# Optimization experiments

Hardware: AMD Instinct MI355X
Metric: run time of the kernel (lower is better)

Reference implementation:

```python
import jax, jax.numpy as jnp
import numpy as np

HEADS = 4
KS = 7  # neighborhood window size


def group_norm(x, g, b, eps=1e-5):
    # GroupNorm(1, C) on NCHW: normalize over (C,H,W) per sample
    mu = x.mean(axis=(1, 2, 3), keepdims=True)
    var = x.var(axis=(1, 2, 3), keepdims=True)
    xn = (x - mu) * jax.lax.rsqrt(var + eps)
    return xn * g[None, :, None, None] + b[None, :, None, None]


def layer_norm(x, g, b, eps=1e-5):
    mu = x.mean(axis=-1, keepdims=True)
    var = x.var(axis=-1, keepdims=True)
    return (x - mu) * jax.lax.rsqrt(var + eps) * g + b


def na2d(x, qkv_w, qkv_b, proj_w, proj_b, rpb):
    # Neighborhood attention 2D (NATTEN semantics: window clamped at borders)
    N, H, W, C = x.shape
    e, k = HEADS, KS
    d = C // e
    qkv = x @ qkv_w.T + qkv_b  # [N,H,W,3C]
    q, kk, v = jnp.split(qkv, 3, axis=-1)
    q = q.reshape(N, H, W, e, d) * (d ** -0.5)
    kk = kk.reshape(N, H, W, e, d)
    v = v.reshape(N, H, W, e, d)
    ni = jnp.clip(jnp.arange(H) - k // 2, 0, H - k)[:, None] + jnp.arange(k)  # [H,k]
    nj = jnp.clip(jnp.arange(W) - k // 2, 0, W - k)[:, None] + jnp.arange(k)  # [W,k]
    kg = kk[:, ni][:, :, :, nj]  # [N,H,i,W,j,e,d]
    vg = v[:, ni][:, :, :, nj]
    scores = jnp.einsum('nhwed,nhiwjed->nhweij', q, kg)  # [N,H,W,e,k,k]
    ri = ni - jnp.arange(H)[:, None] + (k - 1)  # rel pos index in [0, 2k-2]
    rj = nj - jnp.arange(W)[:, None] + (k - 1)
    bias = rpb[:, ri][:, :, :, rj]  # [e,H,i,W,j]
    scores = scores + bias.transpose(1, 3, 0, 2, 4)[None]
    attn = jax.nn.softmax(scores.reshape(N, H, W, e, k * k), axis=-1).reshape(N, H, W, e, k, k)
    out = jnp.einsum('nhweij,nhiwjed->nhwed', attn, vg).reshape(N, H, W, C)
    return out @ proj_w.T + proj_b


def na_layer(x, gn_g, gn_b, qkv_w, qkv_b, proj_w, proj_b, rpb, ln_g, ln_b, fc1_w, fc1_b, fc2_w, fc2_b):
    N, C, H, W = x.shape
    x1 = x.transpose(0, 2, 3, 1)  # n h w c (pre-norm residual)
    xg = group_norm(x, gn_g, gn_b).transpose(0, 2, 3, 1)
    a = na2d(xg, qkv_w, qkv_b, proj_w, proj_b, rpb) + x1
    t = a.reshape(N, H * W, C)
    h = jax.nn.gelu(layer_norm(t, ln_g, ln_b) @ fc1_w.T + fc1_b, approximate=False)
    t = t + (h @ fc2_w.T + fc2_b)
    return t.reshape(N, H, W, C).transpose(0, 3, 1, 2)


def conv3x3(x, w, b):
    y = jax.lax.conv_general_dilated(x, w, (1, 1), 'SAME', dimension_numbers=('NCHW', 'OIHW', 'NCHW'))
    return y + b[None, :, None, None]


def setup_inputs() -> dict:
    key = jax.random.key(0)
    ks = jax.random.split(key, 16)
    N, C, H, W = 2, 128, 64, 64
    L, e, k, hid, red = 2, HEADS, KS, 4 * 128, 18
    rn = lambda kk, shape, s=0.02: jax.random.normal(kk, shape, jnp.float32) * s
    return {
        'x': jax.random.normal(ks[0], (N, C, H, W), jnp.float32),
        'gn_g': jnp.ones((L, C), jnp.float32), 'gn_b': jnp.zeros((L, C), jnp.float32),
        'qkv_w': rn(ks[1], (L, 3 * C, C)), 'qkv_b': jnp.zeros((L, 3 * C), jnp.float32),
        'proj_w': rn(ks[2], (L, C, C)), 'proj_b': jnp.zeros((L, C), jnp.float32),
        'rpb': rn(ks[3], (L, e, 2 * k - 1, 2 * k - 1)),
        'ln_g': jnp.ones((L, C), jnp.float32), 'ln_b': jnp.zeros((L, C), jnp.float32),
        'fc1_w': rn(ks[4], (L, hid, C)), 'fc1_b': jnp.zeros((L, hid), jnp.float32),
        'fc2_w': rn(ks[5], (L, C, hid)), 'fc2_b': jnp.zeros((L, C), jnp.float32),
        'bconv_w': rn(ks[6], (C, C, 3, 3)), 'bconv_b': jnp.zeros((C,), jnp.float32),
        'c1_w': rn(ks[7], (C // 4, C)), 'c1_b': jnp.zeros((C // 4,), jnp.float32),
        'c2_w': rn(ks[8], (C, C // 4)), 'c2_b': jnp.zeros((C,), jnp.float32),
        'ca1_w': rn(ks[9], (C // red, C)), 'ca1_b': jnp.zeros((C // red,), jnp.float32),
        'ca2_w': rn(ks[10], (C, C // red)), 'ca2_b': jnp.zeros((C,), jnp.float32),
    }


def reference(x, gn_g, gn_b, qkv_w, qkv_b, proj_w, proj_b, rpb, ln_g, ln_b, fc1_w, fc1_b, fc2_w, fc2_b, bconv_w, bconv_b, c1_w, c1_b, c2_w, c2_b, ca1_w, ca1_b, ca2_w, ca2_b):
    res = x
    for l in range(gn_g.shape[0]):  # n_resblocks (structurally fixed, small)
        res = na_layer(res, gn_g[l], gn_b[l], qkv_w[l], qkv_b[l], proj_w[l], proj_b[l], rpb[l],
                       ln_g[l], ln_b[l], fc1_w[l], fc1_b[l], fc2_w[l], fc2_b[l])
    res = conv3x3(res, bconv_w, bconv_b)
    # tail: 1x1 conv -> ReLU -> 1x1 conv -> CALayer
    y = jax.nn.relu(jnp.einsum('rc,nchw->nrhw', c1_w, res) + c1_b[None, :, None, None])
    y = jnp.einsum('cr,nrhw->nchw', c2_w, y) + c2_b[None, :, None, None]
    p = y.mean(axis=(2, 3))  # global avg pool -> [N,C]
    s = jax.nn.sigmoid(jax.nn.relu(p @ ca1_w.T + ca1_b) @ ca2_w.T + ca2_b)
    y = y * s[:, :, None, None]
    return y + x
```

## Files before the change

### kernel.cpp

```cpp
#include <hip/hip_runtime.h>
#include <math.h>

typedef unsigned short u16;

#define NN 2
#define CC 128
#define HH 64
#define WW 64
#define NHD 4
#define DH 32
#define KSZ 7
#define PIX (NN*HH*WW)
#define HID 512
#define C4 32
#define CRED 7
#define RW 22
#define RNB 160
#define NBV 154

typedef float f32x4 __attribute__((ext_vector_type(4)));
typedef short bf16x8 __attribute__((ext_vector_type(8)));

static __device__ __forceinline__ float u2f(u16 u){ return __uint_as_float(((unsigned)u) << 16); }
static __device__ __forceinline__ u16 f2u(float f){
    unsigned b = __float_as_uint(f);
    return (u16)((b + 0x7FFFu + ((b >> 16) & 1u)) >> 16);
}

__global__ void detect_k(const u16* __restrict__ x, int* __restrict__ flag,
                         float* __restrict__ poolacc){
    __shared__ float red[256];
    int t = threadIdx.x;
    float mx = 0.f;
    for(int i = t; i < 4096; i += 256){
        float v = fabsf(u2f(x[i]));
        if(v < 1e30f) mx = fmaxf(mx, v);
    }
    red[t] = mx; __syncthreads();
    for(int s = 128; s > 0; s >>= 1){
        if(t < s) red[t] = fmaxf(red[t], red[t+s]);
        __syncthreads();
    }
    if(t == 0) *flag = (red[0] > 1e6f) ? 1 : 0;
    if(t < NN*CC) poolacc[t] = 0.f;
}

struct PtrTab { const void* p[23]; int off[24]; };
#define NCVT 2172
#define NRPK 576
#define NNCH 512

__global__ __launch_bounds__(256) void setup_k(
    PtrTab tab, u16* __restrict__ Wb, u16* __restrict__ Wt,
    const void* __restrict__ convw, const void* __restrict__ x,
    float* __restrict__ cur, float* __restrict__ part,
    const int* __restrict__ flag, int total)
{
    int blk = blockIdx.x;
    int t = threadIdx.x;
    int fl = *flag;
    if(blk < NCVT){
        int i = blk*256 + t;
        if(i < total){
            int a = 0;
            while(i >= tab.off[a+1]) a++;
            int loc = i - tab.off[a];
            Wb[i] = fl ? f2u(((const float*)tab.p[a])[loc]) : ((const u16*)tab.p[a])[loc];
        }
        return;
    }
    if(blk < NCVT + NRPK){
        int i = (blk - NCVT)*256 + t;
        if(i < CC*CC*9){
            int o = i/(9*CC); int rem = i%(9*CC); int tap = rem/CC; int c = rem%CC;
            size_t s = (size_t)(o*CC + c)*9 + tap;
            Wt[i] = fl ? f2u(((const float*)convw)[s]) : ((const u16*)convw)[s];
        }
        return;
    }
    __shared__ float tile[32][65];
    __shared__ float wred[4][2];
    int u = blk - NCVT - NRPK;
    int bx = u & 3, by = u >> 2;
    int n = by >> 6, i = by & 63;
    for(int idx = t; idx < 32*64; idx += 256){
        int cl = idx >> 6, j = idx & 63;
        size_t src = ((size_t)(n*CC + bx*32 + cl)*HH + i)*WW + j;
        tile[cl][j] = fl ? ((const float*)x)[src] : u2f(((const u16*)x)[src]);
    }
    __syncthreads();
    float s = 0.f, q = 0.f;
    for(int idx = t; idx < 64*32; idx += 256){
        int j = idx >> 5, cl = idx & 31;
        float v = tile[cl][j];
        cur[((size_t)((n*HH + i)*WW) + j)*CC + bx*32 + cl] = v;
        s += v; q += v*v;
    }
    #pragma unroll
    for(int off = 32; off > 0; off >>= 1){ s += __shfl_xor(s, off, 64); q += __shfl_xor(q, off, 64); }
    int wave = t >> 6;
    if((t & 63) == 0){ wred[wave][0] = s; wred[wave][1] = q; }
    __syncthreads();
    if(t == 0){
        float ss = wred[0][0]+wred[1][0]+wred[2][0]+wred[3][0];
        float qq = wred[0][1]+wred[1][1]+wred[2][1]+wred[3][1];
        int pidx = n*256 + i*4 + bx;
        part[pidx*2] = ss; part[pidx*2+1] = qq;
    }
}

enum { EPI_NONE = 0, EPI_RES = 1, EPI_GELU = 2 };
enum { OUT_F32 = 0, OUT_BF16 = 1, OUT_BOTH = 2 };
enum { EX_NONE = 0, EX_STATS = 1 };
#define LDP 136

template<int EPI, int OUTM, int AGN, int EXTRA>
__global__ __launch_bounds__(256) void g64_k(
    const void* __restrict__ Av, const u16* __restrict__ W, const u16* __restrict__ bias,
    const float* __restrict__ R, float* __restrict__ Cf, u16* __restrict__ Cb,
    const u16* __restrict__ gnw, const u16* __restrict__ gnb,
    float* __restrict__ gnpart, int gncount,
    int M, int N, int K)
{
    __shared__ __align__(16) u16 As[64*LDP];
    __shared__ __align__(16) u16 Bs[64*LDP];
    __shared__ float wred[4][2];
    const int bm = blockIdx.y*64, bn = blockIdx.x*64;
    const int t = threadIdx.x;
    const int wave = t >> 6, lane = t & 63;
    const int wm = (wave >> 1)*32, wn = (wave & 1)*32;
    const int lg = lane >> 4, lr = lane & 15;
    const int nsm = bm >> 12;
    f32x4 acc[2][2];
    #pragma unroll
    for(int i = 0; i < 2; i++)
        #pragma unroll
        for(int j = 0; j < 2; j++) acc[i][j] = (f32x4){0.f,0.f,0.f,0.f};

    float gmu = 0.f, grs = 0.f;
    if(AGN){
        float a = 0.f, q = 0.f;
        for(int idx = lane; idx < gncount; idx += 64){
            a += gnpart[(nsm*gncount + idx)*2];
            q += gnpart[(nsm*gncount + idx)*2 + 1];
        }
        #pragma unroll
        for(int off = 32; off > 0; off >>= 1){
            a += __shfl_xor(a, off, 64); q += __shfl_xor(q, off, 64);
        }
        const float inv = 1.f/(float)(HH*WW*CC);
        gmu = a*inv;
        grs = rsqrtf(fmaxf(q*inv - gmu*gmu, 0.f) + 1e-5f);
    }

    for(int k0 = 0; k0 < K; k0 += 128){
        uint4 ra[4], rb[4];
        float4 fa[4][2];
        #pragma unroll
        for(int r = 0; r < 4; r++){
            int e = r*256 + t;
            int row = e >> 4, ch = e & 15;
            if(AGN){
                const float* ap = (const float*)Av + (size_t)(bm+row)*K + k0 + ch*8;
                fa[r][0] = *(const float4*)ap;
                fa[r][1] = *(const float4*)(ap + 4);
            } else {
                ra[r] = *(const uint4*)((const u16*)Av + (size_t)(bm+row)*K + k0 + ch*8);
            }
            rb[r] = (bn+row < N) ? *(const uint4*)(W + (size_t)(bn+row)*K + k0 + ch*8)
                                 : (uint4){0,0,0,0};
        }
        #pragma unroll
        for(int r = 0; r < 4; r++){
            int e = r*256 + t;
            int row = e >> 4, ch = e & 15;
            if(AGN){
                union { uint4 u; u16 h[8]; } g8, b8, o8;
                g8.u = *(const uint4*)(gnw + k0 + ch*8);
                b8.u = *(const uint4*)(gnb + k0 + ch*8);
                const float* fv = (const float*)&fa[r][0];
                #pragma unroll
                for(int z = 0; z < 8; z++)
                    o8.h[z] = f2u((fv[z]-gmu)*grs*u2f(g8.h[z]) + u2f(b8.h[z]));
                *(uint4*)&As[row*LDP + ch*8] = o8.u;
            } else {
                *(uint4*)&As[row*LDP + ch*8] = ra[r];
            }
            *(uint4*)&Bs[row*LDP + ch*8] = rb[r];
        }
        __syncthreads();
        #pragma unroll
        for(int kc = 0; kc < 4; kc++){
            bf16x8 af0 = *(const bf16x8*)&As[(wm + lr)*LDP      + kc*32 + lg*8];
            bf16x8 af1 = *(const bf16x8*)&As[(wm + 16 + lr)*LDP + kc*32 + lg*8];
            bf16x8 bf0 = *(const bf16x8*)&Bs[(wn + lr)*LDP      + kc*32 + lg*8];
            bf16x8 bf1 = *(const bf16x8*)&Bs[(wn + 16 + lr)*LDP + kc*32 + lg*8];
            acc[0][0] = __builtin_amdgcn_mfma_f32_16x16x32_bf16(af0, bf0, acc[0][0], 0, 0, 0);
            acc[0][1] = __builtin_amdgcn_mfma_f32_16x16x32_bf16(af0, bf1, acc[0][1], 0, 0, 0);
            acc[1][0] = __builtin_amdgcn_mfma_f32_16x16x32_bf16(af1, bf0, acc[1][0], 0, 0, 0);
            acc[1][1] = __builtin_amdgcn_mfma_f32_16x16x32_bf16(af1, bf1, acc[1][1], 0, 0, 0);
        }
        if(k0 + 128 < K) __syncthreads();
    }

    float ssum = 0.f, sq = 0.f;
    #pragma unroll
    for(int i = 0; i < 2; i++){
        #pragma unroll
        for(int j = 0; j < 2; j++){
            int col = bn + wn + j*16 + lr;
            if(col >= N) continue;
            #pragma unroll
            for(int reg = 0; reg < 4; reg++){
                int row = bm + wm + i*16 + lg*4 + reg;
                float v = acc[i][j][reg] + u2f(bias[col]);
                if(EPI == EPI_RES)  v += R[(size_t)row*N + col];
                if(EPI == EPI_GELU) v = 0.5f*v*(1.f + erff(v*0.70710678118f));
                if(OUTM == OUT_F32 || OUTM == OUT_BOTH) Cf[(size_t)row*N + col] = v;
                if(OUTM == OUT_BF16 || OUTM == OUT_BOTH) Cb[(size_t)row*N + col] = f2u(v);
                if(EXTRA == EX_STATS){ ssum += v; sq += v*v; }
            }
        }
    }
    if(EXTRA == EX_STATS){
        #pragma unroll
        for(int off = 32; off > 0; off >>= 1){
            ssum += __shfl_xor(ssum, off, 64); sq += __shfl_xor(sq, off, 64);
        }
        if(lane == 0){ wred[wave][0] = ssum; wred[wave][1] = sq; }
        __syncthreads();
        if(t == 0){
            int bidx = blockIdx.y*gridDim.x + blockIdx.x;
            gnpart[bidx*2]   = wred[0][0]+wred[1][0]+wred[2][0]+wred[3][0];
            gnpart[bidx*2+1] = wred[0][1]+wred[1][1]+wred[2][1]+wred[3][1];
        }
    }
}

__global__ __launch_bounds__(256) void proj_ln_k(
    const u16* __restrict__ A, const u16* __restrict__ W, const u16* __restrict__ bias,
    const float* __restrict__ R, const u16* __restrict__ lng, const u16* __restrict__ lnb,
    float* __restrict__ abuf, u16* __restrict__ lnout)
{
    __shared__ __align__(16) u16 As[32*LDP];
    __shared__ __align__(16) u16 Bs[128*LDP];
    __shared__ float redS[32][2], redQ[32][2], muS[32], rsS[32];
    const int bm = blockIdx.x*32;
    const int t = threadIdx.x;
    const int wave = t >> 6, lane = t & 63;
    const int wm = (wave >> 1)*16, wn = (wave & 1)*64;
    const int lg = lane >> 4, lr = lane & 15;

    {
        uint4 ra[2], rb[8];
        #pragma unroll
        for(int r = 0; r < 2; r++){
            int e = r*256 + t; int row = e >> 4, ch = e & 15;
            ra[r] = *(const uint4*)(A + (size_t)(bm+row)*CC + ch*8);
        }
        #pragma unroll
        for(int r = 0; r < 8; r++){
            int e = r*256 + t; int row = e >> 4, ch = e & 15;
            rb[r] = *(const uint4*)(W + (size_t)row*CC + ch*8);
        }
        #pragma unroll
        for(int r = 0; r < 2; r++){
            int e = r*256 + t; int row = e >> 4, ch = e & 15;
            *(uint4*)&As[row*LDP + ch*8] = ra[r];
        }
        #pragma unroll
        for(int r = 0; r < 8; r++){
            int e = r*256 + t; int row = e >> 4, ch = e & 15;
            *(uint4*)&Bs[row*LDP + ch*8] = rb[r];
        }
    }
    __syncthreads();

    f32x4 acc[4];
    #pragma unroll
    for(int j = 0; j < 4; j++) acc[j] = (f32x4){0.f,0.f,0.f,0.f};
    #pragma unroll
    for(int kc = 0; kc < 4; kc++){
        bf16x8 af = *(const bf16x8*)&As[(wm + lr)*LDP + kc*32 + lg*8];
        #pragma unroll
        for(int j = 0; j < 4; j++){
            bf16x8 bf = *(const bf16x8*)&Bs[(wn + j*16 + lr)*LDP + kc*32 + lg*8];
            acc[j] = __builtin_amdgcn_mfma_f32_16x16x32_bf16(af, bf, acc[j], 0, 0, 0);
        }
    }
    #pragma unroll
    for(int reg = 0; reg < 4; reg++){
        int rl = wm + lg*4 + reg;
        float rs_ = 0.f, rq_ = 0.f;
        #pragma unroll
        for(int j = 0; j < 4; j++){
            int col = wn + j*16 + lr;
            float v = acc[j][reg] + u2f(bias[col]) + R[(size_t)(bm+rl)*CC + col];
            acc[j][reg] = v;
            abuf[(size_t)(bm+rl)*CC + col] = v;
            rs_ += v; rq_ += v*v;
        }
        rs_ += __shfl_xor(rs_, 1, 64); rq_ += __shfl_xor(rq_, 1, 64);
        rs_ += __shfl_xor(rs_, 2, 64); rq_ += __shfl_xor(rq_, 2, 64);
        rs_ += __shfl_xor(rs_, 4, 64); rq_ += __shfl_xor(rq_, 4, 64);
        rs_ += __shfl_xor(rs_, 8, 64); rq_ += __shfl_xor(rq_, 8, 64);
        if(lr == 0){ redS[rl][wn>>6] = rs_; redQ[rl][wn>>6] = rq_; }
    }
    __syncthreads();
    if(t < 32){
        float mu = (redS[t][0] + redS[t][1])*(1.f/CC);
        float var = fmaxf((redQ[t][0] + redQ[t][1])*(1.f/CC) - mu*mu, 0.f);
        muS[t] = mu; rsS[t] = rsqrtf(var + 1e-5f);
    }
    __syncthreads();
    #pragma unroll
    for(int reg = 0; reg < 4; reg++){
        int rl = wm + lg*4 + reg;
        float mu = muS[rl], rstd = rsS[rl];
        #pragma unroll
        for(int j = 0; j < 4; j++){
            int col = wn + j*16 + lr;
            float v = (acc[j][reg] - mu)*rstd*u2f(lng[col]) + u2f(lnb[col]);
            lnout[(size_t)(bm+rl)*CC + col] = f2u(v);
        }
    }
}

__global__ __launch_bounds__(256) void mct_k(
    const u16* __restrict__ in, const u16* __restrict__ Wt, const u16* __restrict__ bias,
    const u16* __restrict__ c1w, const u16* __restrict__ c1b,
    const u16* __restrict__ c2w, const u16* __restrict__ c2b,
    float* __restrict__ ybuf, float* __restrict__ poolacc)
{
    __shared__ __align__(16) u16 As[16*LDP];
    __shared__ __align__(16) u16 Bs[128*LDP];
    u16* Bs1 = Bs;
    u16* Bs2 = Bs + 32*LDP;
    u16* Hs  = Bs + 32*LDP + 128*40;
    const int bm = blockIdx.x*16;
    const int t = threadIdx.x;
    const int wave = t >> 6, lane = t & 63;
    const int wn = wave*32;
    const int lg = lane >> 4, lr = lane & 15;
    const int nsm = bm >> 12;

    uint4 rb1[2], rb2[2];
    #pragma unroll
    for(int r = 0; r < 2; r++){
        int e = r*256 + t; int row = e >> 4, ch = e & 15;
        rb1[r] = *(const uint4*)(c1w + (size_t)row*CC + ch*8);
    }
    #pragma unroll
    for(int r = 0; r < 2; r++){
        int e = r*256 + t; int row = e >> 2, ch = e & 3;
        rb2[r] = *(const uint4*)(c2w + (size_t)row*C4 + ch*8);
    }

    f32x4 acc[2];
    acc[0] = (f32x4){0.f,0.f,0.f,0.f}; acc[1] = (f32x4){0.f,0.f,0.f,0.f};

    for(int tap = 0; tap < 9; tap++){
        int dy = tap/3 - 1, dx = tap%3 - 1;
        uint4 ra, rb[8];
        {
            int row = t >> 4, ch = t & 15;
            int p = bm + row;
            int n = p >> 12, ii = (p & 4095) >> 6, jj = p & 63;
            int y = ii + dy, x = jj + dx;
            ra = (uint4){0,0,0,0};
            if(y >= 0 && y < HH && x >= 0 && x < WW)
                ra = *(const uint4*)(in + (size_t)(((n*HH + y)*WW + x))*CC + ch*8);
        }
        #pragma unroll
        for(int r = 0; r < 8; r++){
            int e = r*256 + t; int row = e >> 4, ch = e & 15;
            rb[r] = *(const uint4*)(Wt + (size_t)row*(9*CC) + tap*128 + ch*8);
        }
        {
            int row = t >> 4, ch = t & 15;
            *(uint4*)&As[row*LDP + ch*8] = ra;
        }
        #pragma unroll
        for(int r = 0; r < 8; r++){
            int e = r*256 + t; int row = e >> 4, ch = e & 15;
            *(uint4*)&Bs[row*LDP + ch*8] = rb[r];
        }
        __syncthreads();
        #pragma unroll
        for(int kc = 0; kc < 4; kc++){
            bf16x8 af = *(const bf16x8*)&As[lr*LDP + kc*32 + lg*8];
            #pragma unroll
            for(int j = 0; j < 2; j++){
                bf16x8 bf = *(const bf16x8*)&Bs[(wn + j*16 + lr)*LDP + kc*32 + lg*8];
                acc[j] = __builtin_amdgcn_mfma_f32_16x16x32_bf16(af, bf, acc[j], 0, 0, 0);
            }
        }
        __syncthreads();
    }

    #pragma unroll
    for(int j = 0; j < 2; j++){
        int col = wn + j*16 + lr;
        #pragma unroll
        for(int reg = 0; reg < 4; reg++){
            int rl = lg*4 + reg;
            As[rl*LDP + col] = f2u(acc[j][reg] + u2f(bias[col]));
        }
    }
    #pragma unroll
    for(int r = 0; r < 2; r++){
        int e = r*256 + t; int row = e >> 4, ch = e & 15;
        *(uint4*)&Bs1[row*LDP + ch*8] = rb1[r];
    }
    #pragma unroll
    for(int r = 0; r < 2; r++){
        int e = r*256 + t; int row = e >> 2, ch = e & 3;
        *(uint4*)&Bs2[row*40 + ch*8] = rb2[r];
    }
    __syncthreads();

    {
        const int wn1 = (wave & 1)*16;
        f32x4 a1 = (f32x4){0.f,0.f,0.f,0.f};
        #pragma unroll
        for(int kc = 0; kc < 4; kc++){
            bf16x8 af = *(const bf16x8*)&As[lr*LDP + kc*32 + lg*8];
            bf16x8 bf = *(const bf16x8*)&Bs1[(wn1 + lr)*LDP + kc*32 + lg*8];
            a1 = __builtin_amdgcn_mfma_f32_16x16x32_bf16(af, bf, a1, 0, 0, 0);
        }
        #pragma unroll
        for(int reg = 0; reg < 4; reg++){
            int rl = lg*4 + reg;
            int col = wn1 + lr;
            Hs[rl*40 + col] = f2u(fmaxf(a1[reg] + u2f(c1b[col]), 0.f));
        }
    }
    __syncthreads();

    {
        f32x4 a2[2];
        a2[0] = (f32x4){0.f,0.f,0.f,0.f}; a2[1] = (f32x4){0.f,0.f,0.f,0.f};
        bf16x8 af = *(const bf16x8*)&Hs[lr*40 + lg*8];
        #pragma unroll
        for(int j = 0; j < 2; j++){
            bf16x8 bf = *(const bf16x8*)&Bs2[(wn + j*16 + lr)*40 + lg*8];
            a2[j] = __builtin_amdgcn_mfma_f32_16x16x32_bf16(af, bf, a2[j], 0, 0, 0);
        }
        float cs[2] = {0.f, 0.f};
        #pragma unroll
        for(int j = 0; j < 2; j++){
            int col = wn + j*16 + lr;
            #pragma unroll
            for(int reg = 0; reg < 4; reg++){
                int row = bm + lg*4 + reg;
                float v = a2[j][reg] + u2f(c2b[col]);
                ybuf[(size_t)row*CC + col] = v;
                cs[j] += v;
            }
        }
        #pragma unroll
        for(int j = 0; j < 2; j++){
            cs[j] += __shfl_xor(cs[j], 16, 64);
            cs[j] += __shfl_xor(cs[j], 32, 64);
        }
        if(lg == 0){
            #pragma unroll
            for(int j = 0; j < 2; j++)
                atomicAdd(&poolacc[nsm*CC + wn + j*16 + lr], cs[j]);
        }
    }
}

#define KVP 72
#define PSP 168

__global__ __launch_bounds__(128) void att_tile_k(
    const u16* __restrict__ qkv, const u16* __restrict__ rpb, u16* __restrict__ out)
{
    __shared__ __align__(16) u16 KV[2][RNB][KVP];
    __shared__ __align__(16) u16 Qs[16][64];
    __shared__ float rpbs[2][169];
    u16* PsB = &KV[0][0][0];
    const int blk = blockIdx.x;
    const int rb = blk >> 1, eg = blk & 1;
    const int p0 = rb*16;
    const int jb = p0 & 63, i = (p0 >> 6) & 63, n = p0 >> 12;
    const int i0 = min(max(i-3, 0), HH-KSZ);
    const int rc0 = min(max(jb-3, 0), WW-KSZ);
    const int t = threadIdx.x;

    for(int idx = t; idx < 2*169; idx += 128)
        rpbs[idx/169][idx%169] = u2f(rpb[(eg*2 + idx/169)*169 + idx%169]);
    {
        int pix = t >> 3, ch = t & 7;
        *(uint4*)&Qs[pix][ch*8] = *(const uint4*)(qkv + (size_t)(p0+pix)*(3*CC) + eg*64 + ch*8);
    }
    for(int idx = t; idx < RNB*16; idx += 128){
        int nb = idx >> 4, part = idx & 15;
        int kv = part >> 3, ch = part & 7;
        uint4 v = (uint4){0,0,0,0};
        if(nb < NBV){
            int ky = nb/RW, kcol = nb - ky*RW;
            int sy = i0 + ky, sx = min(rc0 + kcol, WW-1);
            v = *(const uint4*)(qkv + (size_t)((n*HH + sy)*WW + sx)*(3*CC) + CC + kv*CC + eg*64 + ch*8);
        }
        *(uint4*)&KV[kv][nb][ch*8] = v;
    }
    __syncthreads();

    const int el = t >> 6;
    const int lane = t & 63, lg = lane >> 4, lr = lane & 15;

    bf16x8 aq = *(const bf16x8*)&Qs[lr][el*32 + lg*8];
    f32x4 sc[10];
    #pragma unroll
    for(int c = 0; c < 10; c++){
        bf16x8 bk = *(const bf16x8*)&KV[0][c*16+lr][el*32 + lg*8];
        sc[c] = __builtin_amdgcn_mfma_f32_16x16x32_bf16(aq, bk, (f32x4){0.f,0.f,0.f,0.f}, 0, 0, 0);
    }
    __syncthreads();
    #pragma unroll
    for(int reg = 0; reg < 4; reg++){
        int pix = lg*4 + reg;
        int j = jb + pix;
        int base = min(max(j-3, 0), WW-KSZ) - rc0;
        float mx = -1e30f;
        #pragma unroll
        for(int c = 0; c < 10; c++){
            int nb = c*16 + lr;
            int ky = nb/RW, kcol = nb - ky*RW;
            float v = -1e30f;
            if(nb < NBV && kcol >= base && kcol <= base+6){
                int ri = i0 + ky - i + (KSZ-1);
                int rj = rc0 + kcol - j + (KSZ-1);
                v = sc[c][reg]*0.17677669529663689f + rpbs[el][ri*13 + rj];
            }
            sc[c][reg] = v;
            mx = fmaxf(mx, v);
        }
        mx = fmaxf(mx, __shfl_xor(mx, 1, 64));
        mx = fmaxf(mx, __shfl_xor(mx, 2, 64));
        mx = fmaxf(mx, __shfl_xor(mx, 4, 64));
        mx = fmaxf(mx, __shfl_xor(mx, 8, 64));
        float sum = 0.f;
        #pragma unroll
        for(int c = 0; c < 10; c++){
            float p = __expf(sc[c][reg] - mx);
            sc[c][reg] = p; sum += p;
        }
        sum += __shfl_xor(sum, 1, 64);
        sum += __shfl_xor(sum, 2, 64);
        sum += __shfl_xor(sum, 4, 64);
        sum += __shfl_xor(sum, 8, 64);
        float rs = 1.f/sum;
        #pragma unroll
        for(int c = 0; c < 10; c++)
            PsB[(el*16 + pix)*PSP + c*16 + lr] = f2u(sc[c][reg]*rs);
    }
    __syncthreads();
    f32x4 o0 = (f32x4){0.f,0.f,0.f,0.f}, o1 = (f32x4){0.f,0.f,0.f,0.f};
    #pragma unroll
    for(int ks = 0; ks < 5; ks++){
        bf16x8 ap = *(const bf16x8*)&PsB[(el*16 + lr)*PSP + ks*32 + lg*8];
        bf16x8 b0, b1;
        #pragma unroll
        for(int jj = 0; jj < 8; jj++){
            int nb = ks*32 + lg*8 + jj;
            b0[jj] = (short)KV[1][nb][el*32 + lr];
            b1[jj] = (short)KV[1][nb][el*32 + 16 + lr];
        }
        o0 = __builtin_amdgcn_mfma_f32_16x16x32_bf16(ap, b0, o0, 0, 0, 0);
        o1 = __builtin_amdgcn_mfma_f32_16x16x32_bf16(ap, b1, o1, 0, 0, 0);
    }
    int e = eg*2 + el;
    #pragma unroll
    for(int reg = 0; reg < 4; reg++){
        int pix = lg*4 + reg;
        out[(size_t)(p0+pix)*CC + e*32 + lr]      = f2u(o0[reg]);
        out[(size_t)(p0+pix)*CC + e*32 + 16 + lr] = f2u(o1[reg]);
    }
}

__global__ __launch_bounds__(256) void final_ca_k(
    const float* __restrict__ y, const float* __restrict__ poolacc,
    const u16* __restrict__ w1, const u16* __restrict__ b1,
    const u16* __restrict__ w2, const u16* __restrict__ b2,
    const void* __restrict__ xraw, void* __restrict__ outv,
    const int* __restrict__ flag)
{
    __shared__ float t1s[CRED];
    __shared__ float sres;
    int id0 = blockIdx.x*256;
    int c = (id0 >> 12) & (CC-1);
    int n = id0 >> 19;
    int t = threadIdx.x;
    if(t < CRED){
        float a = u2f(b1[t]);
        const float pscale = 1.f/(float)(HH*WW);
        for(int cc = 0; cc < CC; cc++)
            a += poolacc[n*CC + cc]*pscale*u2f(w1[t*CC + cc]);
        t1s[t] = fmaxf(a, 0.f);
    }
    __syncthreads();
    if(t == 0){
        float a = u2f(b2[c]);
        #pragma unroll
        for(int r = 0; r < CRED; r++) a += t1s[r]*u2f(w2[c*CRED + r]);
        sres = 1.f/(1.f + __expf(-a));
    }
    __syncthreads();
    float s = sres;
    int id = id0 + t;
    int j = id & 63; int i = (id >> 6) & 63;
    float xr = (*flag) ? ((const float*)xraw)[id] : u2f(((const u16*)xraw)[id]);
    float v = y[(size_t)((n*HH + i)*WW + j)*CC + c]*s + xr;
    if(*flag) ((float*)outv)[id] = v;
    else      ((u16*)outv)[id] = f2u(v);
}

extern "C" void kernel_launch(void* const* d_in, const int* in_sizes, int n_in,
                              void* d_out, int out_size, void* d_ws, size_t ws_size,
                              hipStream_t stream){
    float* wsf    = (float*)d_ws;
    int*   flagp  = (int*)d_ws;
    float* gnpart = wsf + 8;
    float* poolacc= wsf + 1040;

    u16* Wb = (u16*)(wsf + 2048);
    static const int wsizes[23] = {256,256,98304,768,32768,256,1352,256,256,131072,1024,
                                   131072,256,147456,128,4096,32,4096,128,896,7,896,128};
    int woff[24]; woff[0] = 0;
    for(int i = 0; i < 23; i++) woff[i+1] = woff[i] + wsizes[i];
    const int WTOT = woff[23];
    u16* Wt = Wb + 555760;

    float* AB    = wsf + 360448;
    float* cur   = AB;
    u16*  cur16  = (u16*)(AB + 1048576);
    u16*  xg16   = (u16*)(AB + 1572864);
    u16*  qkv16  = (u16*)(AB + 2097152);
    float* abuf  = AB + 2097152;
    u16*  hbuf16 = (u16*)(AB + 3670016);
    float* ybuf  = AB + 3670016;

    detect_k<<<1, 256, 0, stream>>>((const u16*)d_in[0], flagp, poolacc);

    PtrTab tab;
    for(int i = 0; i < 23; i++){ tab.p[i] = d_in[i+1]; tab.off[i] = woff[i]; }
    tab.off[23] = woff[23];
    setup_k<<<NCVT + NRPK + NNCH, 256, 0, stream>>>(
        tab, Wb, Wt, d_in[14], d_in[0], cur, gnpart, flagp, WTOT);

    const u16 *gng = Wb+woff[0], *gnb = Wb+woff[1], *qkvw = Wb+woff[2], *qkvb = Wb+woff[3],
              *projw = Wb+woff[4], *projb = Wb+woff[5], *rpbw = Wb+woff[6], *lng = Wb+woff[7],
              *lnb = Wb+woff[8], *f1w = Wb+woff[9], *f1b = Wb+woff[10], *f2w = Wb+woff[11],
              *f2b = Wb+woff[12], *bcb = Wb+woff[14], *c1w = Wb+woff[15],
              *c1b = Wb+woff[16], *c2w = Wb+woff[17], *c2b = Wb+woff[18], *ca1w = Wb+woff[19],
              *ca1b = Wb+woff[20], *ca2w = Wb+woff[21], *ca2b = Wb+woff[22];

    for(int l = 0; l < 2; l++){
        int gncount = (l == 0) ? 256 : 128;

        g64_k<EPI_NONE,OUT_BF16,1,EX_NONE><<<dim3(6, PIX/64), 256, 0, stream>>>(
            cur, qkvw + (size_t)l*3*CC*CC, qkvb + l*3*CC, nullptr, nullptr, qkv16,
            gng + l*CC, gnb + l*CC, gnpart, gncount, PIX, 3*CC, CC);

        att_tile_k<<<PIX/16*2, 128, 0, stream>>>(qkv16, rpbw + l*NHD*169, xg16);

        proj_ln_k<<<PIX/32, 256, 0, stream>>>(
            xg16, projw + (size_t)l*CC*CC, projb + l*CC, cur, lng + l*CC, lnb + l*CC,
            abuf, xg16);

        g64_k<EPI_GELU,OUT_BF16,0,EX_NONE><<<dim3(8, PIX/64), 256, 0, stream>>>(
            xg16, f1w + (size_t)l*HID*CC, f1b + l*HID, nullptr, nullptr, hbuf16,
            nullptr, nullptr, nullptr, 0, PIX, HID, CC);

        g64_k<EPI_RES,OUT_BOTH,0,EX_STATS><<<dim3(2, PIX/64), 256, 0, stream>>>(
            hbuf16, f2w + (size_t)l*CC*HID, f2b + l*CC, abuf, cur, cur16,
            nullptr, nullptr, gnpart, 0, PIX, CC, HID);
    }

    mct_k<<<PIX/16, 256, 0, stream>>>(cur16, Wt, bcb, c1w, c1b, c2w, c2b, ybuf, poolacc);

    final_ca_k<<<(NN*CC*HH*WW)/256, 256, 0, stream>>>(
        ybuf, poolacc, ca1w, ca1b, ca2w, ca2b, d_in[0], d_out, flagp);
}
```

Baseline: 263.6 us.

## Fold input-format detection into setup kernel and add smaller-tile fc2 GEMM kernel

Removes the separate single-block detect kernel by having every setup block recompute the bf16/f32 flag from the first 256 input elements with a wave reduction. Block 0 writes the flag and zeroes the pool accumulator. The fc2 GEMM moves to a dedicated kernel with 32x64 tiles, which doubles the grid to raise occupancy for the K=512 reduction. That kernel fuses the residual add, the dual f32/bf16 outputs and the GroupNorm partial statistics, so the per-layer GN count is now always 256. The risks are a redundant per-block reduction in setup, a flag that now depends on only 256 samples instead of 4096, and a smaller tile that reuses less data from LDS.

After: 268.4 us. No clear change (+1.8%).

```diff
diff --git a/kernel.cpp b/kernel.cpp
--- a/kernel.cpp
+++ b/kernel.cpp
@@ -27,24 +27,6 @@
     return (u16)((b + 0x7FFFu + ((b >> 16) & 1u)) >> 16);
 }
 
-__global__ void detect_k(const u16* __restrict__ x, int* __restrict__ flag,
-                         float* __restrict__ poolacc){
-    __shared__ float red[256];
-    int t = threadIdx.x;
-    float mx = 0.f;
-    for(int i = t; i < 4096; i += 256){
-        float v = fabsf(u2f(x[i]));
-        if(v < 1e30f) mx = fmaxf(mx, v);
-    }
-    red[t] = mx; __syncthreads();
-    for(int s = 128; s > 0; s >>= 1){
-        if(t < s) red[t] = fmaxf(red[t], red[t+s]);
-        __syncthreads();
-    }
-    if(t == 0) *flag = (red[0] > 1e6f) ? 1 : 0;
-    if(t < NN*CC) poolacc[t] = 0.f;
-}
-
 struct PtrTab { const void* p[23]; int off[24]; };
 #define NCVT 2172
 #define NRPK 576
@@ -54,11 +36,25 @@
     PtrTab tab, u16* __restrict__ Wb, u16* __restrict__ Wt,
     const void* __restrict__ convw, const void* __restrict__ x,
     float* __restrict__ cur, float* __restrict__ part,
-    const int* __restrict__ flag, int total)
+    int* __restrict__ flagp, float* __restrict__ poolacc, int total)
 {
-    int blk = blockIdx.x;
-    int t = threadIdx.x;
-    int fl = *flag;
+    __shared__ float red4[4];
+    const int blk = blockIdx.x, t = threadIdx.x;
+
+    {
+        float v = fabsf(u2f(((const u16*)x)[t]));
+        float mx = (v < 1e30f) ? v : 0.f;
+        #pragma unroll
+        for(int off = 32; off > 0; off >>= 1) mx = fmaxf(mx, __shfl_xor(mx, off, 64));
+        if((t & 63) == 0) red4[t >> 6] = mx;
+    }
+    __syncthreads();
+    const int fl = (fmaxf(fmaxf(red4[0], red4[1]), fmaxf(red4[2], red4[3])) > 1e6f) ? 1 : 0;
+    if(blk == 0){
+        if(t == 0) *flagp = fl;
+        if(t < NN*CC) poolacc[t] = 0.f;
+    }
+
     if(blk < NCVT){
         int i = blk*256 + t;
         if(i < total){
@@ -203,7 +199,6 @@
         if(k0 + 128 < K) __syncthreads();
     }
 
-    float ssum = 0.f, sq = 0.f;
     #pragma unroll
     for(int i = 0; i < 2; i++){
         #pragma unroll
@@ -218,22 +213,87 @@
                 if(EPI == EPI_GELU) v = 0.5f*v*(1.f + erff(v*0.70710678118f));
                 if(OUTM == OUT_F32 || OUTM == OUT_BOTH) Cf[(size_t)row*N + col] = v;
                 if(OUTM == OUT_BF16 || OUTM == OUT_BOTH) Cb[(size_t)row*N + col] = f2u(v);
-                if(EXTRA == EX_STATS){ ssum += v; sq += v*v; }
             }
         }
     }
-    if(EXTRA == EX_STATS){
-        #pragma unroll
-        for(int off = 32; off > 0; off >>= 1){
-            ssum += __shfl_xor(ssum, off, 64); sq += __shfl_xor(sq, off, 64);
-        }
-        if(lane == 0){ wred[wave][0] = ssum; wred[wave][1] = sq; }
+    (void)wred;
+}
+
+__global__ __launch_bounds__(256) void fc2_k(
+    const u16* __restrict__ A, const u16* __restrict__ W, const u16* __restrict__ bias,
+    const float* __restrict__ R, float* __restrict__ Cf, u16* __restrict__ Cb,
+    float* __restrict__ gnpart)
+{
+    __shared__ __align__(16) u16 As[32*LDP];
+    __shared__ __align__(16) u16 Bs[64*LDP];
+    __shared__ float wred[4][2];
+    const int bm = blockIdx.y*32, bn = blockIdx.x*64;
+    const int t = threadIdx.x;
+    const int wave = t >> 6, lane = t & 63;
+    const int wm = (wave >> 1)*16, wn = (wave & 1)*32;
+    const int lg = lane >> 4, lr = lane & 15;
+    const int nsm = bm >> 12;
+    f32x4 acc[2];
+    acc[0] = (f32x4){0.f,0.f,0.f,0.f}; acc[1] = (f32x4){0.f,0.f,0.f,0.f};
+
+    for(int k0 = 0; k0 < HID; k0 += 128){
+        uint4 ra[2], rb[4];
+        #pragma unroll
+        for(int r = 0; r < 2; r++){
+            int e = r*256 + t; int row = e >> 4, ch = e & 15;
+            ra[r] = *(const uint4*)(A + (size_t)(bm+row)*HID + k0 + ch*8);
+        }
+        #pragma unroll
+        for(int r = 0; r < 4; r++){
+            int e = r*256 + t; int row = e >> 4, ch = e & 15;
+            rb[r] = *(const uint4*)(W + (size_t)(bn+row)*HID + k0 + ch*8);
+        }
+        #pragma unroll
+        for(int r = 0; r < 2; r++){
+            int e = r*256 + t; int row = e >> 4, ch = e & 15;
+            *(uint4*)&As[row*LDP + ch*8] = ra[r];
+        }
+        #pragma unroll
+        for(int r = 0; r < 4; r++){
+            int e = r*256 + t; int row = e >> 4, ch = e & 15;
+            *(uint4*)&Bs[row*LDP + ch*8] = rb[r];
+        }
         __syncthreads();
-        if(t == 0){
-            int bidx = blockIdx.y*gridDim.x + blockIdx.x;
-            gnpart[bidx*2]   = wred[0][0]+wred[1][0]+wred[2][0]+wred[3][0];
-            gnpart[bidx*2+1] = wred[0][1]+wred[1][1]+wred[2][1]+wred[3][1];
-        }
+        #pragma unroll
+        for(int kc = 0; kc < 4; kc++){
+            bf16x8 af = *(const bf16x8*)&As[(wm + lr)*LDP + kc*32 + lg*8];
+            #pragma unroll
+            for(int j = 0; j < 2; j++){
+                bf16x8 bf = *(const bf16x8*)&Bs[(wn + j*16 + lr)*LDP + kc*32 + lg*8];
+                acc[j] = __builtin_amdgcn_mfma_f32_16x16x32_bf16(af, bf, acc[j], 0, 0, 0);
+            }
+        }
+        if(k0 + 128 < HID) __syncthreads();
+    }
+
+    float ssum = 0.f, sq = 0.f;
+    #pragma unroll
+    for(int j = 0; j < 2; j++){
+        int col = bn + wn + j*16 + lr;
+        #pragma unroll
+        for(int reg = 0; reg < 4; reg++){
+            int row = bm + wm + lg*4 + reg;
+            float v = acc[j][reg] + u2f(bias[col]) + R[(size_t)row*CC + col];
+            Cf[(size_t)row*CC + col] = v;
+            Cb[(size_t)row*CC + col] = f2u(v);
+            ssum += v; sq += v*v;
+        }
+    }
+    #pragma unroll
+    for(int off = 32; off > 0; off >>= 1){
+        ssum += __shfl_xor(ssum, off, 64); sq += __shfl_xor(sq, off, 64);
+    }
+    if(lane == 0){ wred[wave][0] = ssum; wred[wave][1] = sq; }
+    __syncthreads();
+    if(t == 0){
+        int bidx = blockIdx.y*gridDim.x + blockIdx.x;
+        gnpart[bidx*2]   = wred[0][0]+wred[1][0]+wred[2][0]+wred[3][0];
+        gnpart[bidx*2+1] = wred[0][1]+wred[1][1]+wred[2][1]+wred[3][1];
     }
 }
 
@@ -643,13 +703,11 @@
     u16*  hbuf16 = (u16*)(AB + 3670016);
     float* ybuf  = AB + 3670016;
 
-    detect_k<<<1, 256, 0, stream>>>((const u16*)d_in[0], flagp, poolacc);
-
     PtrTab tab;
     for(int i = 0; i < 23; i++){ tab.p[i] = d_in[i+1]; tab.off[i] = woff[i]; }
     tab.off[23] = woff[23];
     setup_k<<<NCVT + NRPK + NNCH, 256, 0, stream>>>(
-        tab, Wb, Wt, d_in[14], d_in[0], cur, gnpart, flagp, WTOT);
+        tab, Wb, Wt, d_in[14], d_in[0], cur, gnpart, flagp, poolacc, WTOT);
 
     const u16 *gng = Wb+woff[0], *gnb = Wb+woff[1], *qkvw = Wb+woff[2], *qkvb = Wb+woff[3],
               *projw = Wb+woff[4], *projb = Wb+woff[5], *rpbw = Wb+woff[6], *lng = Wb+woff[7],
@@ -659,11 +717,9 @@
               *ca1b = Wb+woff[20], *ca2w = Wb+woff[21], *ca2b = Wb+woff[22];
 
     for(int l = 0; l < 2; l++){
-        int gncount = (l == 0) ? 256 : 128;
-
         g64_k<EPI_NONE,OUT_BF16,1,EX_NONE><<<dim3(6, PIX/64), 256, 0, stream>>>(
             cur, qkvw + (size_t)l*3*CC*CC, qkvb + l*3*CC, nullptr, nullptr, qkv16,
-            gng + l*CC, gnb + l*CC, gnpart, gncount, PIX, 3*CC, CC);
+            gng + l*CC, gnb + l*CC, gnpart, 256, PIX, 3*CC, CC);
 
         att_tile_k<<<PIX/16*2, 128, 0, stream>>>(qkv16, rpbw + l*NHD*169, xg16);
 
@@ -675,9 +731,8 @@
             xg16, f1w + (size_t)l*HID*CC, f1b + l*HID, nullptr, nullptr, hbuf16,
             nullptr, nullptr, nullptr, 0, PIX, HID, CC);
 
-        g64_k<EPI_RES,OUT_BOTH,0,EX_STATS><<<dim3(2, PIX/64), 256, 0, stream>>>(
-            hbuf16, f2w + (size_t)l*CC*HID, f2b + l*CC, abuf, cur, cur16,
-            nullptr, nullptr, gnpart, 0, PIX, CC, HID);
+        fc2_k<<<dim3(2, PIX/32), 256, 0, stream>>>(
+            hbuf16, f2w + (size_t)l*CC*HID, f2b + l*CC, abuf, cur, cur16, gnpart);
     }
 
     mct_k<<<PIX/16, 256, 0, stream>>>(cur16, Wt, bcb, c1w, c1b, c2w, c2b, ybuf, poolacc);
```
